# Kernel optimization log

Measured on AMD Instinct MI355X. Metric: run time of the kernel, lower is better.

## Reference

```python
import jax, jax.numpy as jnp
import numpy as np

EMBED_DIM = 1024
NUM_HEADS = 16
HEAD_DIM = EMBED_DIM // NUM_HEADS


def setup_inputs() -> dict:
    key = jax.random.key(0)
    ks = jax.random.split(key, 9)
    B, S, E = 4, 2048, EMBED_DIM
    # xavier_uniform bound for square [E, E] weights
    bound = float(np.sqrt(6.0 / (E + E)))
    def w(k):
        return jax.random.uniform(k, (E, E), jnp.float32, -bound, bound)
    return {
        "x": jax.random.normal(ks[0], (B, S, E), jnp.float32),
        "Wq": w(ks[1]), "bq": jnp.zeros((E,), jnp.float32),
        "Wk": w(ks[2]), "bk": jnp.zeros((E,), jnp.float32),
        "Wv": w(ks[3]), "bv": jnp.zeros((E,), jnp.float32),
        "Wo": w(ks[4]), "bo": jnp.zeros((E,), jnp.float32),
    }


def reference(x, Wq, bq, Wk, bk, Wv, bv, Wo, bo):
    B, S, E = x.shape
    H, D = NUM_HEADS, HEAD_DIM
    # Linear projections (torch Linear: x @ W.T + b)
    q = (x @ Wq.T + bq).reshape(B, S, H, D)
    k = (x @ Wk.T + bk).reshape(B, S, H, D)
    v = (x @ Wv.T + bv).reshape(B, S, H, D)
    # per-head scaled dot-product attention (vectorized over heads)
    scores = jnp.einsum("bqhd,bkhd->bhqk", q, k) / jnp.sqrt(jnp.float32(D))
    attn = jax.nn.softmax(scores, axis=-1)
    o = jnp.einsum("bhqk,bkhd->bqhd", attn, v).reshape(B, S, E)
    return o @ Wo.T + bo
```

## Files before the change

### kernel.cpp

```cpp
#include <hip/hip_runtime.h>
#include <stdint.h>

typedef unsigned short u16;
typedef short bf16x8 __attribute__((ext_vector_type(8)));
typedef float f32x4 __attribute__((ext_vector_type(4)));

#define B_ 4
#define S_ 2048
#define H_ 16
#define D_ 64
#define E_ 1024
#define M_ (B_ * S_)

static __device__ __forceinline__ u16 f2bf(float f) {
  uint32_t u = __builtin_bit_cast(uint32_t, f);
  u += 0x7fffu + ((u >> 16) & 1u);
  return (u16)(u >> 16);
}
static __device__ __forceinline__ u16 hu16(float f) {
  return (u16)((__builtin_bit_cast(uint32_t, f) + 0x8000u) >> 16);
}
static __device__ __forceinline__ uint32_t pack2bf(float a, float b) {
  return (uint32_t)f2bf(a) | ((uint32_t)f2bf(b) << 16);
}

static __device__ __forceinline__ void gld_lds16(const void* g, void* l) {
  __builtin_amdgcn_global_load_lds(
      (const __attribute__((address_space(1))) void*)(uintptr_t)g,
      (__attribute__((address_space(3))) void*)(uint32_t)(uintptr_t)l, 16, 0, 0);
}

template <int ctrl>
static __device__ __forceinline__ float dpp_mov(float x) {
  return __builtin_bit_cast(float,
      __builtin_amdgcn_update_dpp(0, __builtin_bit_cast(int, x), ctrl, 0xF, 0xF, true));
}
static __device__ __forceinline__ float rowsum16(float x) {
  x += dpp_mov<0xB1>(x);
  x += dpp_mov<0x4E>(x);
  x += dpp_mov<0x141>(x);
  x += dpp_mov<0x140>(x);
  return x;
}

__global__ __launch_bounds__(256) void cvt_f32_bf16(const float* __restrict__ in,
                                                    u16* __restrict__ out, int n) {
  int i = (blockIdx.x * 256 + threadIdx.x) * 8;
  if (i + 8 > n) return;
  float4 a = *(const float4*)(in + i);
  float4 b = *(const float4*)(in + i + 4);
  struct __align__(16) U8 { u16 h[8]; } u;
  u.h[0] = f2bf(a.x); u.h[1] = f2bf(a.y); u.h[2] = f2bf(a.z); u.h[3] = f2bf(a.w);
  u.h[4] = f2bf(b.x); u.h[5] = f2bf(b.y); u.h[6] = f2bf(b.z); u.h[7] = f2bf(b.w);
  *(U8*)(out + i) = u;
}

template <int KIND, typename OutT>
static __device__ __forceinline__ void gemm128(const u16* __restrict__ A,
                                               const u16* __restrict__ W,
                                               const float* __restrict__ bias,
                                               OutT* __restrict__ C, int m0, int n0,
                                               float scale, u16* As, u16* Bs) {
  const int tid = threadIdx.x;
  const int wave = tid >> 6, lane = tid & 63;
  const int col16 = lane & 15, quad = lane >> 4;
  const int wm = wave >> 1, wn = wave & 1;

  f32x4 acc[4][4] = {};

  const int r0 = tid >> 3;
  const int sg8 = ((tid & 7) ^ (r0 & 7)) * 8;
  const u16* ga = A + (size_t)(m0 + r0) * E_ + sg8;
  const u16* gb = W + (size_t)(n0 + r0) * E_ + sg8;
  u16* lA = As + wave * 512;
  u16* lB = Bs + wave * 512;

  for (int k0 = 0; k0 < E_; k0 += 64) {
    __syncthreads();
#pragma unroll
    for (int i = 0; i < 4; i++) {
      gld_lds16(ga + (size_t)(i * 32) * E_ + k0, lA + i * 2048);
      gld_lds16(gb + (size_t)(i * 32) * E_ + k0, lB + i * 2048);
    }
    asm volatile("s_waitcnt vmcnt(0)" ::: "memory");
    __syncthreads();

    bf16x8 af[4][2], bw[4][2];
#pragma unroll
    for (int mt = 0; mt < 4; mt++)
#pragma unroll
      for (int ks = 0; ks < 2; ks++)
        af[mt][ks] = *(const bf16x8*)&As[(wm * 64 + mt * 16 + col16) * 64 +
                                         (((ks * 4 + quad) ^ (col16 & 7)) * 8)];
#pragma unroll
    for (int nt = 0; nt < 4; nt++)
#pragma unroll
      for (int ks = 0; ks < 2; ks++)
        bw[nt][ks] = *(const bf16x8*)&Bs[(wn * 64 + nt * 16 + col16) * 64 +
                                         (((ks * 4 + quad) ^ (col16 & 7)) * 8)];
#pragma unroll
    for (int ks = 0; ks < 2; ks++)
#pragma unroll
      for (int a = 0; a < 4; a++)
#pragma unroll
        for (int b = 0; b < 4; b++) {
          if constexpr (KIND == 2)
            acc[a][b] = __builtin_amdgcn_mfma_f32_16x16x32_bf16(af[a][ks], bw[b][ks], acc[a][b], 0, 0, 0);
          else
            acc[a][b] = __builtin_amdgcn_mfma_f32_16x16x32_bf16(bw[a][ks], af[b][ks], acc[a][b], 0, 0, 0);
        }
  }

  if constexpr (KIND == 2) {
#pragma unroll
    for (int a = 0; a < 4; a++) {
      int t = m0 + wm * 64 + a * 16 + quad * 4;
      int bb = t >> 11, s = t & (S_ - 1);
#pragma unroll
      for (int b = 0; b < 4; b++) {
        int oc = n0 + wn * 64 + b * 16 + col16;
        int h = oc >> 6, d = oc & 63;
        float bv = bias[oc];
        uint32_t lo = pack2bf(acc[a][b][0] + bv, acc[a][b][1] + bv);
        uint32_t hi = pack2bf(acc[a][b][2] + bv, acc[a][b][3] + bv);
        uint2 pk = {lo, hi};
        *(uint2*)&C[(((size_t)(bb * H_ + h) * D_ + d) * S_) + s] = pk;
      }
    }
  } else {
#pragma unroll
    for (int b = 0; b < 4; b++) {
      int row = m0 + wm * 64 + b * 16 + col16;
#pragma unroll
      for (int a = 0; a < 4; a++) {
        int nc = n0 + wn * 64 + a * 16 + quad * 4;
        float4 bv = *(const float4*)&bias[nc];
        float v0 = (acc[a][b][0] + bv.x) * scale;
        float v1 = (acc[a][b][1] + bv.y) * scale;
        float v2 = (acc[a][b][2] + bv.z) * scale;
        float v3 = (acc[a][b][3] + bv.w) * scale;
        if constexpr (KIND == 0) {
          uint2 pk = {pack2bf(v0, v1), pack2bf(v2, v3)};
          *(uint2*)&((u16*)C)[(size_t)row * E_ + nc] = pk;
        } else {
          float4 pk = {v0, v1, v2, v3};
          *(float4*)&((float*)C)[(size_t)row * E_ + nc] = pk;
        }
      }
    }
  }
}

__global__ __launch_bounds__(256) void gemm_qkv(const u16* __restrict__ xb,
                                                const u16* __restrict__ wq, const u16* __restrict__ wk,
                                                const u16* __restrict__ wv,
                                                const float* __restrict__ bq, const float* __restrict__ bk,
                                                const float* __restrict__ bv,
                                                u16* __restrict__ Qb, u16* __restrict__ Kb,
                                                u16* __restrict__ Vtb) {
  __shared__ __align__(16) u16 As[128 * 64];
  __shared__ __align__(16) u16 Bs[128 * 64];
  const int mat = blockIdx.x >> 3;
  const int n0 = (blockIdx.x & 7) * 128;
  const int m0 = blockIdx.y * 128;
  if (mat == 0)
    gemm128<0, u16>(xb, wq, bq, Qb, m0, n0, 0.125f * 1.44269504f, As, Bs);
  else if (mat == 1)
    gemm128<0, u16>(xb, wk, bk, Kb, m0, n0, 1.0f, As, Bs);
  else
    gemm128<2, u16>(xb, wv, bv, Vtb, m0, n0, 1.0f, As, Bs);
}

__global__ __launch_bounds__(256) void gemm_out(const u16* __restrict__ Ob,
                                                const u16* __restrict__ wob,
                                                const float* __restrict__ bo,
                                                float* __restrict__ out) {
  __shared__ __align__(16) u16 As[128 * 64];
  __shared__ __align__(16) u16 Bs[128 * 64];
  gemm128<1, float>(Ob, wob, bo, out, blockIdx.y * 128, blockIdx.x * 128, 1.0f, As, Bs);
}

__global__ __launch_bounds__(256) void flash_attn(const u16* __restrict__ Q,
                                                  const u16* __restrict__ K,
                                                  const u16* __restrict__ Vt,
                                                  u16* __restrict__ O) {
  __shared__ __align__(16) u16 Ks[2][64 * 64];
  __shared__ __align__(16) u16 Vs[2][64 * 64];
  __shared__ __align__(16) u16 Ps[4][32 * 72];
  const int bid = blockIdx.x;
  const int qt = bid & 15, h = (bid >> 4) & 15, b = bid >> 8;
  const int tid = threadIdx.x;
  const int wave = tid >> 6, lane = tid & 63;
  const int col16 = lane & 15, quad = lane >> 4;

  bf16x8 qf[2][2];
  const int qrow = qt * 128 + wave * 32;
#pragma unroll
  for (int mt = 0; mt < 2; mt++) {
    const u16* qp = Q + ((size_t)(b * S_ + qrow + mt * 16 + col16) * H_ + h) * D_ + quad * 8;
    qf[mt][0] = *(const bf16x8*)qp;
    qf[mt][1] = *(const bf16x8*)(qp + 32);
  }

  f32x4 o_acc[2][4] = {};
  float l_i[2][4] = {};

  const int srow = tid >> 3;
  const int sgrp = (tid & 7) ^ (srow & 7);
  const u16* Kbase = K + ((size_t)(b * S_) * H_ + h) * D_;
  const u16* Vbase = Vt + ((size_t)(b * H_ + h) * D_) * S_;
  u16* Pw = &Ps[wave][0];

  auto stage = [&](int kb, int buf) {
#pragma unroll
    for (int i = 0; i < 2; i++) {
      gld_lds16(Kbase + (size_t)(kb * 64 + i * 32 + srow) * (H_ * D_) + sgrp * 8,
                &Ks[buf][i * 2048 + wave * 512]);
      gld_lds16(Vbase + (size_t)(i * 32 + srow) * S_ + kb * 64 + sgrp * 8,
                &Vs[buf][i * 2048 + wave * 512]);
    }
  };

  stage(0, 0);
  for (int kb = 0; kb < S_ / 64; kb++) {
    const int cur = kb & 1;
    asm volatile("s_waitcnt vmcnt(0)" ::: "memory");
    __syncthreads();
    if (kb + 1 < S_ / 64) stage(kb + 1, cur ^ 1);
    const u16* KsC = Ks[cur];
    const u16* VsC = Vs[cur];

    f32x4 sacc[2][4] = {};
#pragma unroll
    for (int ks = 0; ks < 2; ks++) {
      bf16x8 kf[4];
#pragma unroll
      for (int nt = 0; nt < 4; nt++)
        kf[nt] = *(const bf16x8*)&KsC[(nt * 16 + col16) * 64 +
                                      (((ks * 4 + quad) ^ (col16 & 7)) * 8)];
#pragma unroll
      for (int mt = 0; mt < 2; mt++)
#pragma unroll
        for (int nt = 0; nt < 4; nt++)
          sacc[mt][nt] = __builtin_amdgcn_mfma_f32_16x16x32_bf16(qf[mt][ks], kf[nt], sacc[mt][nt], 0, 0, 0);
    }

#pragma unroll
    for (int mt = 0; mt < 2; mt++) {
#pragma unroll
      for (int e = 0; e < 4; e++) {
        float p0 = __builtin_amdgcn_exp2f(sacc[mt][0][e]);
        float p1 = __builtin_amdgcn_exp2f(sacc[mt][1][e]);
        float p2 = __builtin_amdgcn_exp2f(sacc[mt][2][e]);
        float p3 = __builtin_amdgcn_exp2f(sacc[mt][3][e]);
        l_i[mt][e] += (p0 + p1) + (p2 + p3);
        const int r = mt * 16 + quad * 4 + e;
        const int ro = r * 72;
        const int cb = col16 + ((r & 8) ? 16 : 0);
        Pw[ro + (cb & 63)] = hu16(p0);
        Pw[ro + ((cb + 16) & 63)] = hu16(p1);
        Pw[ro + ((cb + 32) & 63)] = hu16(p2);
        Pw[ro + ((cb + 48) & 63)] = hu16(p3);
      }
    }
    asm volatile("s_waitcnt lgkmcnt(0)" ::: "memory");

#pragma unroll
    for (int ks = 0; ks < 2; ks++) {
      bf16x8 pf[2], vf[4];
#pragma unroll
      for (int mt = 0; mt < 2; mt++)
        pf[mt] = *(const bf16x8*)&Pw[(mt * 16 + col16) * 72 +
                                     (((ks * 4 + quad + ((col16 >> 3) << 1)) & 7) * 8)];
#pragma unroll
      for (int nt = 0; nt < 4; nt++)
        vf[nt] = *(const bf16x8*)&VsC[(nt * 16 + col16) * 64 +
                                      (((ks * 4 + quad) ^ (col16 & 7)) * 8)];
#pragma unroll
      for (int mt = 0; mt < 2; mt++)
#pragma unroll
        for (int nt = 0; nt < 4; nt++)
          o_acc[mt][nt] = __builtin_amdgcn_mfma_f32_16x16x32_bf16(pf[mt], vf[nt], o_acc[mt][nt], 0, 0, 0);
    }
  }

#pragma unroll
  for (int mt = 0; mt < 2; mt++) {
#pragma unroll
    for (int e = 0; e < 4; e++) {
      float inv = 1.f / rowsum16(l_i[mt][e]);
      int s = qrow + mt * 16 + quad * 4 + e;
#pragma unroll
      for (int nt = 0; nt < 4; nt++)
        O[((size_t)(b * S_ + s) * H_ + h) * D_ + nt * 16 + col16] =
            f2bf(o_acc[mt][nt][e] * inv);
    }
  }
}

extern "C" void kernel_launch(void* const* d_in, const int* in_sizes, int n_in,
                              void* d_out, int out_size, void* d_ws, size_t ws_size,
                              hipStream_t stream) {
  (void)in_sizes; (void)n_in; (void)out_size; (void)ws_size;
  const float* x  = (const float*)d_in[0];
  const float* Wq = (const float*)d_in[1];
  const float* bq = (const float*)d_in[2];
  const float* Wk = (const float*)d_in[3];
  const float* bk = (const float*)d_in[4];
  const float* Wv = (const float*)d_in[5];
  const float* bv = (const float*)d_in[6];
  const float* Wo = (const float*)d_in[7];
  const float* bo = (const float*)d_in[8];
  float* out = (float*)d_out;

  const size_t NX = (size_t)M_ * E_;
  const size_t NW = (size_t)E_ * E_;
  u16* xb  = (u16*)d_ws;
  u16* wqb = xb + NX;
  u16* wkb = wqb + NW;
  u16* wvb = wkb + NW;
  u16* wob = wvb + NW;
  u16* Qb  = wob + NW;
  u16* Kb  = Qb + NX;
  u16* Vtb = Kb + NX;
  u16* Ob  = Vtb + NX;

  cvt_f32_bf16<<<NX / 2048, 256, 0, stream>>>(x, xb, (int)NX);
  cvt_f32_bf16<<<NW / 2048, 256, 0, stream>>>(Wq, wqb, (int)NW);
  cvt_f32_bf16<<<NW / 2048, 256, 0, stream>>>(Wk, wkb, (int)NW);
  cvt_f32_bf16<<<NW / 2048, 256, 0, stream>>>(Wv, wvb, (int)NW);
  cvt_f32_bf16<<<NW / 2048, 256, 0, stream>>>(Wo, wob, (int)NW);

  gemm_qkv<<<dim3(24, 64), 256, 0, stream>>>(xb, wqb, wkb, wvb, bq, bk, bv, Qb, Kb, Vtb);
  flash_attn<<<B_ * H_ * (S_ / 128), 256, 0, stream>>>(Qb, Kb, Vtb, Ob);
  gemm_out<<<dim3(8, 64), 256, 0, stream>>>(Ob, wob, bo, out);
}
```

Measured before the change: 303.2 us.

## Enlarge GEMM tiles to 256x256, fuse conversion launches, reorder attention blocks

```diff
diff --git a/kernel.cpp b/kernel.cpp
--- a/kernel.cpp
+++ b/kernel.cpp
@@ -43,20 +43,32 @@
   return x;
 }
 
-__global__ __launch_bounds__(256) void cvt_f32_bf16(const float* __restrict__ in,
-                                                    u16* __restrict__ out, int n) {
+#define NXE (M_ * E_)
+#define NWE (E_ * E_)
+__global__ __launch_bounds__(256) void cvt_all(const float* __restrict__ x,
+                                               const float* __restrict__ Wq,
+                                               const float* __restrict__ Wk,
+                                               const float* __restrict__ Wv,
+                                               const float* __restrict__ Wo,
+                                               u16* __restrict__ ws) {
   int i = (blockIdx.x * 256 + threadIdx.x) * 8;
-  if (i + 8 > n) return;
-  float4 a = *(const float4*)(in + i);
-  float4 b = *(const float4*)(in + i + 4);
+  const float* src;
+  u16* dst = ws + i;
+  if (i < NXE) { src = x + i; }
+  else if (i < NXE + NWE)     { src = Wq + (i - NXE); }
+  else if (i < NXE + 2 * NWE) { src = Wk + (i - NXE - NWE); }
+  else if (i < NXE + 3 * NWE) { src = Wv + (i - NXE - 2 * NWE); }
+  else                        { src = Wo + (i - NXE - 3 * NWE); }
+  float4 a = *(const float4*)src;
+  float4 b = *(const float4*)(src + 4);
   struct __align__(16) U8 { u16 h[8]; } u;
   u.h[0] = f2bf(a.x); u.h[1] = f2bf(a.y); u.h[2] = f2bf(a.z); u.h[3] = f2bf(a.w);
   u.h[4] = f2bf(b.x); u.h[5] = f2bf(b.y); u.h[6] = f2bf(b.z); u.h[7] = f2bf(b.w);
-  *(U8*)(out + i) = u;
+  *(U8*)dst = u;
 }
 
 template <int KIND, typename OutT>
-static __device__ __forceinline__ void gemm128(const u16* __restrict__ A,
+static __device__ __forceinline__ void gemm256(const u16* __restrict__ A,
                                                const u16* __restrict__ W,
                                                const float* __restrict__ bias,
                                                OutT* __restrict__ C, int m0, int n0,
@@ -64,9 +76,9 @@
   const int tid = threadIdx.x;
   const int wave = tid >> 6, lane = tid & 63;
   const int col16 = lane & 15, quad = lane >> 4;
-  const int wm = wave >> 1, wn = wave & 1;
-
-  f32x4 acc[4][4] = {};
+  const int wm = wave & 3, wn = wave >> 2;
+
+  f32x4 acc[8][4] = {};
 
   const int r0 = tid >> 3;
   const int sg8 = ((tid & 7) ^ (r0 & 7)) * 8;
@@ -79,51 +91,46 @@
     __syncthreads();
 #pragma unroll
     for (int i = 0; i < 4; i++) {
-      gld_lds16(ga + (size_t)(i * 32) * E_ + k0, lA + i * 2048);
-      gld_lds16(gb + (size_t)(i * 32) * E_ + k0, lB + i * 2048);
+      gld_lds16(ga + (size_t)(i * 64) * E_ + k0, lA + i * 4096);
+      gld_lds16(gb + (size_t)(i * 64) * E_ + k0, lB + i * 4096);
     }
     asm volatile("s_waitcnt vmcnt(0)" ::: "memory");
     __syncthreads();
 
-    bf16x8 af[4][2], bw[4][2];
-#pragma unroll
-    for (int mt = 0; mt < 4; mt++)
-#pragma unroll
-      for (int ks = 0; ks < 2; ks++)
-        af[mt][ks] = *(const bf16x8*)&As[(wm * 64 + mt * 16 + col16) * 64 +
-                                         (((ks * 4 + quad) ^ (col16 & 7)) * 8)];
-#pragma unroll
-    for (int nt = 0; nt < 4; nt++)
-#pragma unroll
-      for (int ks = 0; ks < 2; ks++)
-        bw[nt][ks] = *(const bf16x8*)&Bs[(wn * 64 + nt * 16 + col16) * 64 +
-                                         (((ks * 4 + quad) ^ (col16 & 7)) * 8)];
-#pragma unroll
-    for (int ks = 0; ks < 2; ks++)
-#pragma unroll
-      for (int a = 0; a < 4; a++)
+#pragma unroll
+    for (int ks = 0; ks < 2; ks++) {
+      const int ko = ((ks * 4 + quad) ^ (col16 & 7)) * 8;
+      bf16x8 af[4], bw[8];
+#pragma unroll
+      for (int mt = 0; mt < 4; mt++)
+        af[mt] = *(const bf16x8*)&As[(wm * 64 + mt * 16 + col16) * 64 + ko];
+#pragma unroll
+      for (int nt = 0; nt < 8; nt++)
+        bw[nt] = *(const bf16x8*)&Bs[(wn * 128 + nt * 16 + col16) * 64 + ko];
+#pragma unroll
+      for (int a = 0; a < 8; a++)
 #pragma unroll
         for (int b = 0; b < 4; b++) {
           if constexpr (KIND == 2)
-            acc[a][b] = __builtin_amdgcn_mfma_f32_16x16x32_bf16(af[a][ks], bw[b][ks], acc[a][b], 0, 0, 0);
+            acc[a][b] = __builtin_amdgcn_mfma_f32_16x16x32_bf16(af[b], bw[a], acc[a][b], 0, 0, 0);
           else
-            acc[a][b] = __builtin_amdgcn_mfma_f32_16x16x32_bf16(bw[a][ks], af[b][ks], acc[a][b], 0, 0, 0);
+            acc[a][b] = __builtin_amdgcn_mfma_f32_16x16x32_bf16(bw[a], af[b], acc[a][b], 0, 0, 0);
         }
+    }
   }
 
   if constexpr (KIND == 2) {
 #pragma unroll
-    for (int a = 0; a < 4; a++) {
-      int t = m0 + wm * 64 + a * 16 + quad * 4;
+    for (int b = 0; b < 4; b++) {
+      int t = m0 + wm * 64 + b * 16 + quad * 4;
       int bb = t >> 11, s = t & (S_ - 1);
 #pragma unroll
-      for (int b = 0; b < 4; b++) {
-        int oc = n0 + wn * 64 + b * 16 + col16;
+      for (int a = 0; a < 8; a++) {
+        int oc = n0 + wn * 128 + a * 16 + col16;
         int h = oc >> 6, d = oc & 63;
         float bv = bias[oc];
-        uint32_t lo = pack2bf(acc[a][b][0] + bv, acc[a][b][1] + bv);
-        uint32_t hi = pack2bf(acc[a][b][2] + bv, acc[a][b][3] + bv);
-        uint2 pk = {lo, hi};
+        uint2 pk = {pack2bf(acc[a][b][0] + bv, acc[a][b][1] + bv),
+                    pack2bf(acc[a][b][2] + bv, acc[a][b][3] + bv)};
         *(uint2*)&C[(((size_t)(bb * H_ + h) * D_ + d) * S_) + s] = pk;
       }
     }
@@ -132,8 +139,8 @@
     for (int b = 0; b < 4; b++) {
       int row = m0 + wm * 64 + b * 16 + col16;
 #pragma unroll
-      for (int a = 0; a < 4; a++) {
-        int nc = n0 + wn * 64 + a * 16 + quad * 4;
+      for (int a = 0; a < 8; a++) {
+        int nc = n0 + wn * 128 + a * 16 + quad * 4;
         float4 bv = *(const float4*)&bias[nc];
         float v0 = (acc[a][b][0] + bv.x) * scale;
         float v1 = (acc[a][b][1] + bv.y) * scale;
@@ -151,33 +158,33 @@
   }
 }
 
-__global__ __launch_bounds__(256) void gemm_qkv(const u16* __restrict__ xb,
-                                                const u16* __restrict__ wq, const u16* __restrict__ wk,
-                                                const u16* __restrict__ wv,
-                                                const float* __restrict__ bq, const float* __restrict__ bk,
-                                                const float* __restrict__ bv,
-                                                u16* __restrict__ Qb, u16* __restrict__ Kb,
-                                                u16* __restrict__ Vtb) {
-  __shared__ __align__(16) u16 As[128 * 64];
-  __shared__ __align__(16) u16 Bs[128 * 64];
-  const int mat = blockIdx.x >> 3;
-  const int n0 = (blockIdx.x & 7) * 128;
-  const int m0 = blockIdx.y * 128;
+__global__ __launch_bounds__(512, 2) void gemm_qkv(const u16* __restrict__ xb,
+                                                   const u16* __restrict__ wq, const u16* __restrict__ wk,
+                                                   const u16* __restrict__ wv,
+                                                   const float* __restrict__ bq, const float* __restrict__ bk,
+                                                   const float* __restrict__ bv,
+                                                   u16* __restrict__ Qb, u16* __restrict__ Kb,
+                                                   u16* __restrict__ Vtb) {
+  __shared__ __align__(16) u16 As[256 * 64];
+  __shared__ __align__(16) u16 Bs[256 * 64];
+  const int mat = blockIdx.y >> 2;
+  const int n0 = (blockIdx.y & 3) * 256;
+  const int m0 = blockIdx.x * 256;
   if (mat == 0)
-    gemm128<0, u16>(xb, wq, bq, Qb, m0, n0, 0.125f * 1.44269504f, As, Bs);
+    gemm256<0, u16>(xb, wq, bq, Qb, m0, n0, 0.125f * 1.44269504f, As, Bs);
   else if (mat == 1)
-    gemm128<0, u16>(xb, wk, bk, Kb, m0, n0, 1.0f, As, Bs);
+    gemm256<0, u16>(xb, wk, bk, Kb, m0, n0, 1.0f, As, Bs);
   else
-    gemm128<2, u16>(xb, wv, bv, Vtb, m0, n0, 1.0f, As, Bs);
-}
-
-__global__ __launch_bounds__(256) void gemm_out(const u16* __restrict__ Ob,
-                                                const u16* __restrict__ wob,
-                                                const float* __restrict__ bo,
-                                                float* __restrict__ out) {
-  __shared__ __align__(16) u16 As[128 * 64];
-  __shared__ __align__(16) u16 Bs[128 * 64];
-  gemm128<1, float>(Ob, wob, bo, out, blockIdx.y * 128, blockIdx.x * 128, 1.0f, As, Bs);
+    gemm256<2, u16>(xb, wv, bv, Vtb, m0, n0, 1.0f, As, Bs);
+}
+
+__global__ __launch_bounds__(512, 2) void gemm_out(const u16* __restrict__ Ob,
+                                                   const u16* __restrict__ wob,
+                                                   const float* __restrict__ bo,
+                                                   float* __restrict__ out) {
+  __shared__ __align__(16) u16 As[256 * 64];
+  __shared__ __align__(16) u16 Bs[256 * 64];
+  gemm256<1, float>(Ob, wob, bo, out, blockIdx.x * 256, blockIdx.y * 256, 1.0f, As, Bs);
 }
 
 __global__ __launch_bounds__(256) void flash_attn(const u16* __restrict__ Q,
@@ -188,7 +195,7 @@
   __shared__ __align__(16) u16 Vs[2][64 * 64];
   __shared__ __align__(16) u16 Ps[4][32 * 72];
   const int bid = blockIdx.x;
-  const int qt = bid & 15, h = (bid >> 4) & 15, b = bid >> 8;
+  const int qt = bid >> 6, h = bid & 15, b = (bid >> 4) & 3;
   const int tid = threadIdx.x;
   const int wave = tid >> 6, lane = tid & 63;
   const int col16 = lane & 15, quad = lane >> 4;
@@ -325,13 +332,9 @@
   u16* Vtb = Kb + NX;
   u16* Ob  = Vtb + NX;
 
-  cvt_f32_bf16<<<NX / 2048, 256, 0, stream>>>(x, xb, (int)NX);
-  cvt_f32_bf16<<<NW / 2048, 256, 0, stream>>>(Wq, wqb, (int)NW);
-  cvt_f32_bf16<<<NW / 2048, 256, 0, stream>>>(Wk, wkb, (int)NW);
-  cvt_f32_bf16<<<NW / 2048, 256, 0, stream>>>(Wv, wvb, (int)NW);
-  cvt_f32_bf16<<<NW / 2048, 256, 0, stream>>>(Wo, wob, (int)NW);
-
-  gemm_qkv<<<dim3(24, 64), 256, 0, stream>>>(xb, wqb, wkb, wvb, bq, bk, bv, Qb, Kb, Vtb);
+  cvt_all<<<(NX + 4 * NW) / 2048, 256, 0, stream>>>(x, Wq, Wk, Wv, Wo, xb);
+
+  gemm_qkv<<<dim3(32, 12), 512, 0, stream>>>(xb, wqb, wkb, wvb, bq, bk, bv, Qb, Kb, Vtb);
   flash_attn<<<B_ * H_ * (S_ / 128), 256, 0, stream>>>(Qb, Kb, Vtb, Ob);
-  gemm_out<<<dim3(8, 64), 256, 0, stream>>>(Ob, wob, bo, out);
-}
+  gemm_out<<<dim3(32, 4), 512, 0, stream>>>(Ob, wob, bo, out);
+}
```

Result: slower. 320.4 us (+5.7%).
